# Kernel optimization log

Hardware: AMD Instinct MI355X
Metric: run time of the kernel (lower is better)

## Reference

```python
import jax, jax.numpy as jnp
import numpy as np

INPUT_DIM = 512
HIDDEN_DIM = 512


def setup_inputs() -> dict:
    key = jax.random.key(0)
    k1, k2 = jax.random.split(key, 2)
    T, B = 2048, 32
    x = jax.random.normal(k1, (T, B, INPUT_DIM), dtype=jnp.float32)
    hidden_state = jnp.zeros((1, B, HIDDEN_DIM), dtype=jnp.float32)
    cell_state = jnp.zeros((1, B, HIDDEN_DIM), dtype=jnp.float32)
    # xavier_uniform for weights, zeros for bias (matches init_weights)
    dim_size = INPUT_DIM + HIDDEN_DIM
    limit = np.sqrt(6.0 / (dim_size + 4 * HIDDEN_DIM)).astype(np.float32)
    weights = jax.random.uniform(k2, (dim_size, 4 * HIDDEN_DIM), dtype=jnp.float32,
                                 minval=-limit, maxval=limit)
    bias = jnp.zeros((4 * HIDDEN_DIM,), dtype=jnp.float32)
    return {"x": x, "hidden_state": hidden_state, "cell_state": cell_state,
            "weights": weights, "bias": bias}


def reference(x, hidden_state, cell_state, weights, bias):
    H = HIDDEN_DIM

    def step(carry, x_t):
        h, c = carry  # [1, B, H] each; x_t: [B, input_dim]
        concat = jnp.concatenate((x_t[None], h), axis=2)  # [1, B, in+H]
        gates = jnp.matmul(concat, weights) + bias        # [1, B, 4H]
        f = jax.nn.sigmoid(gates[:, :, :H])
        i = jax.nn.sigmoid(gates[:, :, H:2 * H])
        g = jnp.tanh(gates[:, :, 2 * H:3 * H])
        o = jax.nn.sigmoid(gates[:, :, 3 * H:])
        c_new = f * c + i * g
        h_new = o * jnp.tanh(c_new)
        return (h_new, c_new), h_new[0]  # emit [B, H]

    (h_f, c_f), outs = jax.lax.scan(step, (hidden_state, cell_state), x)
    return outs, (h_f, c_f)
```

## Files before the change

### kernel.cpp

```cpp
#include <hip/hip_runtime.h>
#include <math.h>

#define T_STEPS 2048
#define BATCH   32
#define IN_DIM  512
#define H_DIM   512
#define G4      2048
#define NWG     16
#define NTHR    512
#define TC      512
#define NCHUNK  4
#define GLS     132

typedef __attribute__((ext_vector_type(8))) short short8;
typedef __attribute__((ext_vector_type(4))) float f32x4;
typedef __attribute__((ext_vector_type(4))) unsigned u32x4;

__device__ inline unsigned short f2bf(float f) {
    unsigned u = __builtin_bit_cast(unsigned, f);
    unsigned r = (u + 0x7FFFu + ((u >> 16) & 1u)) >> 16;
    return (unsigned short)r;
}
__device__ inline unsigned pack2(float a, float b) {
    return (unsigned)f2bf(a) | ((unsigned)f2bf(b) << 16);
}
__device__ inline float sigm(float v) { return 1.f / (1.f + expf(-v)); }

__global__ __launch_bounds__(256) void wt_kernel(const float* __restrict__ W,
                                                 unsigned short* __restrict__ Wt) {
    __shared__ unsigned short tile[32][33];
    const int n0 = blockIdx.x << 5, k0 = blockIdx.y << 5;
    const int tx = threadIdx.x & 31, ty = threadIdx.x >> 5;
    #pragma unroll
    for (int r = 0; r < 32; r += 8)
        tile[ty + r][tx] = f2bf(W[(size_t)(k0 + ty + r) * G4 + n0 + tx]);
    __syncthreads();
    #pragma unroll
    for (int r = 0; r < 32; r += 8)
        Wt[(size_t)(n0 + ty + r) * 1024 + k0 + tx] = tile[tx][ty + r];
}

__global__ void init_h(const float* __restrict__ h0, unsigned short* __restrict__ hb) {
    int i = blockIdx.x * 256 + threadIdx.x;
    hb[i] = f2bf(h0[i]);
}

__global__ __launch_bounds__(256) void xw_mfma(const float* __restrict__ x,
                                               const unsigned short* __restrict__ Wt,
                                               const float* __restrict__ bias,
                                               float* __restrict__ pre) {
    __shared__ unsigned short As[64][40];
    __shared__ unsigned short Bs[64][40];
    const int tid = threadIdx.x;
    const int w = tid >> 6, l = tid & 63;
    const int m0 = blockIdx.y << 6, n0 = blockIdx.x << 6;
    const int srow = tid >> 2, sseg = (tid & 3) << 3;
    const int arow = (w << 4) + (l & 15);
    const int kb = (l >> 4) << 3;
    f32x4 acc[4] = {};

    for (int kc = 0; kc < 16; ++kc) {
        const float* xs = x + (size_t)(m0 + srow) * IN_DIM + kc * 32 + sseg;
        float4 xa = *(const float4*)xs;
        float4 xb2 = *(const float4*)(xs + 4);
        int4 av;
        av.x = pack2(xa.x, xa.y);  av.y = pack2(xa.z, xa.w);
        av.z = pack2(xb2.x, xb2.y); av.w = pack2(xb2.z, xb2.w);
        *(int4*)&As[srow][sseg] = av;
        *(int4*)&Bs[srow][sseg] = *(const int4*)(Wt + (size_t)(n0 + srow) * 1024 + kc * 32 + sseg);
        __syncthreads();
        short8 af = *(const short8*)&As[arow][kb];
        #pragma unroll
        for (int n = 0; n < 4; ++n) {
            short8 bf = *(const short8*)&Bs[(n << 4) + (l & 15)][kb];
            acc[n] = __builtin_amdgcn_mfma_f32_16x16x32_bf16(af, bf, acc[n], 0, 0, 0);
        }
        __syncthreads();
    }
    #pragma unroll
    for (int n = 0; n < 4; ++n) {
        const int col = n0 + (n << 4) + (l & 15);
        const float bb = bias[col];
        #pragma unroll
        for (int ri = 0; ri < 4; ++ri) {
            const int row = m0 + (w << 4) + ((l >> 4) << 2) + ri;
            pre[(size_t)row * G4 + col] = acc[n][ri] + bb;
        }
    }
}

__global__ __launch_bounds__(NTHR, 2) void lstm_scan(
        const unsigned short* __restrict__ Wt,
        const float* __restrict__ pre,
        const float* __restrict__ cin,
        float* __restrict__ cout,
        unsigned short* __restrict__ hbuf,
        float* __restrict__ outs,
        float* __restrict__ hf, float* __restrict__ cf,
        unsigned int* __restrict__ bar,
        int gt0) {
    __shared__ char Hl[32768];
    const int g = blockIdx.x;
    const int tid = threadIdx.x;
    const int w = tid >> 6, l = tid & 63;

    const int gc = ((w >> 1) << 9) + (g << 5) + ((w & 1) << 4) + (l & 15);
    short8 wf[16];
    #pragma unroll
    for (int kc = 0; kc < 16; ++kc)
        wf[kc] = *(const short8*)(Wt + (size_t)gc * 1024 + 512 + kc * 32 + ((l >> 4) << 3));

    const int b   = tid >> 4;
    const int hcp = (tid & 15) << 1;
    const int col = (g << 5) + hcp;
    float2 cv = *(const float2*)(cin + (b << 9) + col);

    const int arow0 = l & 15, arow1 = (l & 15) + 16;
    const int kbyte = (l >> 4) << 4;
    const int lcw = (w << 4) + (l & 15);
    const char* HlRd0 = Hl + arow0 * 1024;
    const char* HlRd1 = Hl + arow1 * 1024;
    const int swz0 = (arow0 & 7) << 4, swz1 = (arow1 & 7) << 4;
    __syncthreads();

    for (int t = 0; t < TC; ++t) {
        const int gt = gt0 + t;

        const float* pr = pre + ((size_t)t * BATCH + b) * G4 + col;
        const float2 pf = *(const float2*)pr;
        const float2 pi = *(const float2*)(pr + 512);
        const float2 pg = *(const float2*)(pr + 1024);
        const float2 po = *(const float2*)(pr + 1536);

        {
            const unsigned short* hsrc = hbuf + ((gt & 1) << 14);
            const unsigned short* hp0 = hsrc + (w << 9) + (l << 3);
            u32x4 v0, v1, v2, v3;
            asm volatile(
                "global_load_dwordx4 %0, %4, off sc1\n\t"
                "global_load_dwordx4 %1, %5, off sc1\n\t"
                "global_load_dwordx4 %2, %6, off sc1\n\t"
                "global_load_dwordx4 %3, %7, off sc1\n\t"
                "s_waitcnt vmcnt(0)"
                : "=&v"(v0), "=&v"(v1), "=&v"(v2), "=&v"(v3)
                : "v"(hp0), "v"(hp0 + 4096), "v"(hp0 + 8192), "v"(hp0 + 12288)
                : "memory");
            char* ld = Hl + w * 1024 + ((l << 4) ^ (w << 4));
            *(u32x4*)(ld)         = v0;
            *(u32x4*)(ld + 8192)  = v1;
            *(u32x4*)(ld + 16384) = v2;
            *(u32x4*)(ld + 24576) = v3;
        }
        __syncthreads();

        f32x4 acc0 = {0.f, 0.f, 0.f, 0.f}, acc1 = {0.f, 0.f, 0.f, 0.f};
        #pragma unroll
        for (int kc = 0; kc < 16; ++kc) {
            const int kb2 = kc * 64 + kbyte;
            short8 a0 = *(const short8*)(HlRd0 + (kb2 ^ swz0));
            short8 a1 = *(const short8*)(HlRd1 + (kb2 ^ swz1));
            acc0 = __builtin_amdgcn_mfma_f32_16x16x32_bf16(a0, wf[kc], acc0, 0, 0, 0);
            acc1 = __builtin_amdgcn_mfma_f32_16x16x32_bf16(a1, wf[kc], acc1, 0, 0, 0);
        }
        __syncthreads();
        float* Gl = (float*)Hl;
        #pragma unroll
        for (int ri = 0; ri < 4; ++ri) {
            const int br = ((l >> 4) << 2) + ri;
            Gl[br * GLS + lcw] = acc0[ri];
            Gl[(br + 16) * GLS + lcw] = acc1[ri];
        }
        __syncthreads();

        const float* grow = Gl + b * GLS + hcp;
        const float f0 = sigm(grow[0]  + pf.x), f1 = sigm(grow[1]  + pf.y);
        const float i0 = sigm(grow[32] + pi.x), i1 = sigm(grow[33] + pi.y);
        const float g0 = tanhf(grow[64] + pg.x), g1 = tanhf(grow[65] + pg.y);
        const float o0 = sigm(grow[96] + po.x), o1 = sigm(grow[97] + po.y);
        cv.x = f0 * cv.x + i0 * g0;
        cv.y = f1 * cv.y + i1 * g1;
        const float hn0 = o0 * tanhf(cv.x);
        const float hn1 = o1 * tanhf(cv.y);

        *(float2*)(outs + (size_t)gt * (BATCH * H_DIM) + (b << 9) + col) =
            make_float2(hn0, hn1);
        {
            unsigned* hdst = (unsigned*)(hbuf + (((gt + 1) & 1) << 14)) + (((b << 9) + col) >> 1);
            const unsigned pk = pack2(hn0, hn1);
            asm volatile("global_store_dword %0, %1, off sc1" :: "v"(hdst), "v"(pk) : "memory");
        }
        if (gt == T_STEPS - 1) {
            *(float2*)(hf + (b << 9) + col) = make_float2(hn0, hn1);
            *(float2*)(cf + (b << 9) + col) = make_float2(cv.x, cv.y);
        }

        asm volatile("s_waitcnt vmcnt(0)" ::: "memory");
        __syncthreads();
        if (tid == 0) {
            atomicAdd(bar, 1u);
            const unsigned tgt = (unsigned)(gt + 1) * NWG;
            for (;;) {
                unsigned vb;
                asm volatile("global_load_dword %0, %1, off sc1\n\ts_waitcnt vmcnt(0)"
                             : "=v"(vb) : "v"(bar) : "memory");
                if (vb >= tgt) break;
                __builtin_amdgcn_s_sleep(1);
            }
        }
        __syncthreads();
    }

    cout[(b << 9) + col]     = cv.x;
    cout[(b << 9) + col + 1] = cv.y;
}

__global__ __launch_bounds__(256) void lstm_step(const float* __restrict__ x_t,
                                                 const float* __restrict__ h_prev,
                                                 const float* __restrict__ W,
                                                 const float* __restrict__ bias,
                                                 const float* __restrict__ c_in,
                                                 float* __restrict__ c_out,
                                                 float* __restrict__ h_out,
                                                 float* __restrict__ hf,
                                                 float* __restrict__ cf, int last) {
    const int tid = threadIdx.x;
    const int hcc = tid & 7, b = tid >> 3;
    const int col = blockIdx.x * 8 + hcc;
    float a0 = bias[col], a1 = bias[col + 512], a2 = bias[col + 1024], a3 = bias[col + 1536];
    const float* xr = x_t + (size_t)b * IN_DIM;
    const float* hr = h_prev + (size_t)b * H_DIM;
    for (int k = 0; k < IN_DIM; ++k) {
        const float v = xr[k];
        const float* wk = &W[(size_t)k * G4 + col];
        a0 += v * wk[0]; a1 += v * wk[512]; a2 += v * wk[1024]; a3 += v * wk[1536];
    }
    for (int k = 0; k < H_DIM; ++k) {
        const float v = hr[k];
        const float* wk = &W[(size_t)(512 + k) * G4 + col];
        a0 += v * wk[0]; a1 += v * wk[512]; a2 += v * wk[1024]; a3 += v * wk[1536];
    }
    const float cn = sigm(a0) * c_in[(size_t)b * H_DIM + col] + sigm(a1) * tanhf(a2);
    const float hn = sigm(a3) * tanhf(cn);
    c_out[(size_t)b * H_DIM + col] = cn;
    h_out[(size_t)b * H_DIM + col] = hn;
    if (last) { hf[(size_t)b * H_DIM + col] = hn; cf[(size_t)b * H_DIM + col] = cn; }
}

extern "C" void kernel_launch(void* const* d_in, const int* in_sizes, int n_in,
                              void* d_out, int out_size, void* d_ws, size_t ws_size,
                              hipStream_t stream) {
    const float* x    = (const float*)d_in[0];
    const float* h0   = (const float*)d_in[1];
    const float* c0   = (const float*)d_in[2];
    const float* W    = (const float*)d_in[3];
    const float* bias = (const float*)d_in[4];

    float* outs = (float*)d_out;
    float* hf   = outs + (size_t)T_STEPS * BATCH * H_DIM;
    float* cf   = hf + BATCH * H_DIM;

    const size_t OFF_WT  = 134217728ull;
    const size_t OFF_HB  = OFF_WT + 4194304ull;
    const size_t OFF_C   = OFF_HB + 65536ull;
    const size_t OFF_BAR = OFF_C + 65536ull;
    const size_t NEED    = OFF_BAR + 4096ull;

    if (ws_size >= NEED) {
        float* pre = (float*)d_ws;
        unsigned short* Wt = (unsigned short*)((char*)d_ws + OFF_WT);
        unsigned short* hb = (unsigned short*)((char*)d_ws + OFF_HB);
        float* c_ws        = (float*)((char*)d_ws + OFF_C);
        unsigned int* bar  = (unsigned int*)((char*)d_ws + OFF_BAR);

        hipMemsetAsync(bar, 0, 64, stream);
        wt_kernel<<<dim3(64, 32), 256, 0, stream>>>(W, Wt);
        init_h<<<64, 256, 0, stream>>>(h0, hb);
        for (int k = 0; k < NCHUNK; ++k) {
            xw_mfma<<<dim3(32, TC * BATCH / 64), 256, 0, stream>>>(
                x + (size_t)k * TC * BATCH * IN_DIM, Wt, bias, pre);
            lstm_scan<<<NWG, NTHR, 0, stream>>>(
                Wt, pre, (k == 0) ? c0 : c_ws, c_ws, hb, outs, hf, cf, bar, k * TC);
        }
    } else {
        float* c_ws = (float*)d_ws;
        for (int t = 0; t < T_STEPS; ++t) {
            const float* hp = t ? outs + (size_t)(t - 1) * BATCH * H_DIM : h0;
            const float* ci = t ? c_ws : c0;
            lstm_step<<<64, 256, 0, stream>>>(x + (size_t)t * BATCH * IN_DIM,
                                              hp, W, bias, ci, c_ws,
                                              outs + (size_t)t * BATCH * H_DIM,
                                              hf, cf, (t == T_STEPS - 1) ? 1 : 0);
        }
    }
}
```

Baseline: 8.969 ms.

## Fuse input projection into persistent LSTM scan with prefetched bf16 x tiles

Removes the separate xW GEMM and its large fp32 pre-activation buffer. The recurrent kernel now holds both the input and the recurrent weight fragments in registers and does the x_t·W_x MFMAs inside each step. The next step's bf16 x tile is loaded from global memory during the current step and staged into LDS. The scan becomes a single launch over all timesteps instead of four chunks. The cost is doubled MFMA work on the serial critical path and higher register and LDS pressure, with occupancy dropped to one block per CU.

```diff
diff --git a/kernel.cpp b/kernel.cpp
--- a/kernel.cpp
+++ b/kernel.cpp
@@ -8,8 +8,6 @@
 #define G4      2048
 #define NWG     16
 #define NTHR    512
-#define TC      512
-#define NCHUNK  4
 #define GLS     132
 
 typedef __attribute__((ext_vector_type(8))) short short8;
@@ -25,6 +23,19 @@
     return (unsigned)f2bf(a) | ((unsigned)f2bf(b) << 16);
 }
 __device__ inline float sigm(float v) { return 1.f / (1.f + expf(-v)); }
+
+__device__ inline void ld4x_ic(const void* p0, const void* p1,
+                               const void* p2, const void* p3,
+                               u32x4& v0, u32x4& v1, u32x4& v2, u32x4& v3) {
+    asm volatile(
+        "global_load_dwordx4 %0, %4, off sc1\n\t"
+        "global_load_dwordx4 %1, %5, off sc1\n\t"
+        "global_load_dwordx4 %2, %6, off sc1\n\t"
+        "global_load_dwordx4 %3, %7, off sc1\n\t"
+        "s_waitcnt vmcnt(0)"
+        : "=&v"(v0), "=&v"(v1), "=&v"(v2), "=&v"(v3)
+        : "v"(p0), "v"(p1), "v"(p2), "v"(p3) : "memory");
+}
 
 __global__ __launch_bounds__(256) void wt_kernel(const float* __restrict__ W,
                                                  unsigned short* __restrict__ Wt) {
@@ -45,124 +56,97 @@
     hb[i] = f2bf(h0[i]);
 }
 
-__global__ __launch_bounds__(256) void xw_mfma(const float* __restrict__ x,
-                                               const unsigned short* __restrict__ Wt,
-                                               const float* __restrict__ bias,
-                                               float* __restrict__ pre) {
-    __shared__ unsigned short As[64][40];
-    __shared__ unsigned short Bs[64][40];
-    const int tid = threadIdx.x;
-    const int w = tid >> 6, l = tid & 63;
-    const int m0 = blockIdx.y << 6, n0 = blockIdx.x << 6;
-    const int srow = tid >> 2, sseg = (tid & 3) << 3;
-    const int arow = (w << 4) + (l & 15);
-    const int kb = (l >> 4) << 3;
-    f32x4 acc[4] = {};
-
-    for (int kc = 0; kc < 16; ++kc) {
-        const float* xs = x + (size_t)(m0 + srow) * IN_DIM + kc * 32 + sseg;
-        float4 xa = *(const float4*)xs;
-        float4 xb2 = *(const float4*)(xs + 4);
-        int4 av;
-        av.x = pack2(xa.x, xa.y);  av.y = pack2(xa.z, xa.w);
-        av.z = pack2(xb2.x, xb2.y); av.w = pack2(xb2.z, xb2.w);
-        *(int4*)&As[srow][sseg] = av;
-        *(int4*)&Bs[srow][sseg] = *(const int4*)(Wt + (size_t)(n0 + srow) * 1024 + kc * 32 + sseg);
-        __syncthreads();
-        short8 af = *(const short8*)&As[arow][kb];
-        #pragma unroll
-        for (int n = 0; n < 4; ++n) {
-            short8 bf = *(const short8*)&Bs[(n << 4) + (l & 15)][kb];
-            acc[n] = __builtin_amdgcn_mfma_f32_16x16x32_bf16(af, bf, acc[n], 0, 0, 0);
-        }
-        __syncthreads();
-    }
-    #pragma unroll
-    for (int n = 0; n < 4; ++n) {
-        const int col = n0 + (n << 4) + (l & 15);
-        const float bb = bias[col];
-        #pragma unroll
-        for (int ri = 0; ri < 4; ++ri) {
-            const int row = m0 + (w << 4) + ((l >> 4) << 2) + ri;
-            pre[(size_t)row * G4 + col] = acc[n][ri] + bb;
-        }
-    }
-}
-
-__global__ __launch_bounds__(NTHR, 2) void lstm_scan(
+__global__ __launch_bounds__(256) void xb_kernel(const float* __restrict__ x,
+                                                 unsigned short* __restrict__ xb) {
+    const size_t i = ((size_t)blockIdx.x * 256 + threadIdx.x) * 8;
+    const float4 a = *(const float4*)(x + i);
+    const float4 b = *(const float4*)(x + i + 4);
+    u32x4 v;
+    v.x = pack2(a.x, a.y); v.y = pack2(a.z, a.w);
+    v.z = pack2(b.x, b.y); v.w = pack2(b.z, b.w);
+    *(u32x4*)(xb + i) = v;
+}
+
+__global__ __launch_bounds__(NTHR, 1) void lstm_scan(
         const unsigned short* __restrict__ Wt,
-        const float* __restrict__ pre,
-        const float* __restrict__ cin,
-        float* __restrict__ cout,
+        const unsigned short* __restrict__ xb,
+        const float* __restrict__ bias,
+        const float* __restrict__ c0,
         unsigned short* __restrict__ hbuf,
         float* __restrict__ outs,
         float* __restrict__ hf, float* __restrict__ cf,
-        unsigned int* __restrict__ bar,
-        int gt0) {
-    __shared__ char Hl[32768];
+        unsigned int* __restrict__ bar) {
+    __shared__ char LDS_[65536];
+    char* Hl = LDS_;
+    char* Xl = LDS_ + 32768;
+
     const int g = blockIdx.x;
     const int tid = threadIdx.x;
     const int w = tid >> 6, l = tid & 63;
 
     const int gc = ((w >> 1) << 9) + (g << 5) + ((w & 1) << 4) + (l & 15);
-    short8 wf[16];
+    const int ksub = (l >> 4) << 3;
+    short8 wfh[16], wfx[16];
     #pragma unroll
-    for (int kc = 0; kc < 16; ++kc)
-        wf[kc] = *(const short8*)(Wt + (size_t)gc * 1024 + 512 + kc * 32 + ((l >> 4) << 3));
+    for (int kc = 0; kc < 16; ++kc) {
+        wfh[kc] = *(const short8*)(Wt + (size_t)gc * 1024 + 512 + kc * 32 + ksub);
+        wfx[kc] = *(const short8*)(Wt + (size_t)gc * 1024 +       kc * 32 + ksub);
+    }
+    const float bb = bias[gc];
 
     const int b   = tid >> 4;
     const int hcp = (tid & 15) << 1;
     const int col = (g << 5) + hcp;
-    float2 cv = *(const float2*)(cin + (b << 9) + col);
+    float2 cv = *(const float2*)(c0 + (b << 9) + col);
 
     const int arow0 = l & 15, arow1 = (l & 15) + 16;
     const int kbyte = (l >> 4) << 4;
+    const int swz0 = (arow0 & 7) << 4, swz1 = (arow1 & 7) << 4;
     const int lcw = (w << 4) + (l & 15);
-    const char* HlRd0 = Hl + arow0 * 1024;
-    const char* HlRd1 = Hl + arow1 * 1024;
-    const int swz0 = (arow0 & 7) << 4, swz1 = (arow1 & 7) << 4;
+
+    {
+        const u32x4* xsrc = (const u32x4*)xb;
+        u32x4 p0 = xsrc[(w << 6) + l], p1 = xsrc[(w << 6) + l + 512];
+        u32x4 p2 = xsrc[(w << 6) + l + 1024], p3 = xsrc[(w << 6) + l + 1536];
+        char* xd = Xl + w * 1024 + ((l << 4) ^ (w << 4));
+        *(u32x4*)xd = p0; *(u32x4*)(xd + 8192) = p1;
+        *(u32x4*)(xd + 16384) = p2; *(u32x4*)(xd + 24576) = p3;
+
+        const unsigned short* hp0 = hbuf + (w << 9) + (l << 3);
+        u32x4 v0, v1, v2, v3;
+        ld4x_ic(hp0, hp0 + 4096, hp0 + 8192, hp0 + 12288, v0, v1, v2, v3);
+        char* hd = Hl + w * 1024 + ((l << 4) ^ (w << 4));
+        *(u32x4*)hd = v0; *(u32x4*)(hd + 8192) = v1;
+        *(u32x4*)(hd + 16384) = v2; *(u32x4*)(hd + 24576) = v3;
+    }
     __syncthreads();
 
-    for (int t = 0; t < TC; ++t) {
-        const int gt = gt0 + t;
-
-        const float* pr = pre + ((size_t)t * BATCH + b) * G4 + col;
-        const float2 pf = *(const float2*)pr;
-        const float2 pi = *(const float2*)(pr + 512);
-        const float2 pg = *(const float2*)(pr + 1024);
-        const float2 po = *(const float2*)(pr + 1536);
-
-        {
-            const unsigned short* hsrc = hbuf + ((gt & 1) << 14);
-            const unsigned short* hp0 = hsrc + (w << 9) + (l << 3);
-            u32x4 v0, v1, v2, v3;
-            asm volatile(
-                "global_load_dwordx4 %0, %4, off sc1\n\t"
-                "global_load_dwordx4 %1, %5, off sc1\n\t"
-                "global_load_dwordx4 %2, %6, off sc1\n\t"
-                "global_load_dwordx4 %3, %7, off sc1\n\t"
-                "s_waitcnt vmcnt(0)"
-                : "=&v"(v0), "=&v"(v1), "=&v"(v2), "=&v"(v3)
-                : "v"(hp0), "v"(hp0 + 4096), "v"(hp0 + 8192), "v"(hp0 + 12288)
-                : "memory");
-            char* ld = Hl + w * 1024 + ((l << 4) ^ (w << 4));
-            *(u32x4*)(ld)         = v0;
-            *(u32x4*)(ld + 8192)  = v1;
-            *(u32x4*)(ld + 16384) = v2;
-            *(u32x4*)(ld + 24576) = v3;
-        }
-        __syncthreads();
-
-        f32x4 acc0 = {0.f, 0.f, 0.f, 0.f}, acc1 = {0.f, 0.f, 0.f, 0.f};
+    for (int gt = 0; gt < T_STEPS; ++gt) {
+        const int gtn = (gt < T_STEPS - 1) ? gt + 1 : gt;
+        const u32x4* xsrc = (const u32x4*)(xb + ((size_t)gtn << 14));
+        const u32x4 px0 = xsrc[(w << 6) + l];
+        const u32x4 px1 = xsrc[(w << 6) + l + 512];
+        const u32x4 px2 = xsrc[(w << 6) + l + 1024];
+        const u32x4 px3 = xsrc[(w << 6) + l + 1536];
+
+        f32x4 ah0 = {bb, bb, bb, bb}, ah1 = {bb, bb, bb, bb};
+        f32x4 ax0 = {0.f, 0.f, 0.f, 0.f}, ax1 = {0.f, 0.f, 0.f, 0.f};
         #pragma unroll
         for (int kc = 0; kc < 16; ++kc) {
             const int kb2 = kc * 64 + kbyte;
-            short8 a0 = *(const short8*)(HlRd0 + (kb2 ^ swz0));
-            short8 a1 = *(const short8*)(HlRd1 + (kb2 ^ swz1));
-            acc0 = __builtin_amdgcn_mfma_f32_16x16x32_bf16(a0, wf[kc], acc0, 0, 0, 0);
-            acc1 = __builtin_amdgcn_mfma_f32_16x16x32_bf16(a1, wf[kc], acc1, 0, 0, 0);
-        }
-        __syncthreads();
+            short8 ha0 = *(const short8*)(Hl + arow0 * 1024 + (kb2 ^ swz0));
+            short8 ha1 = *(const short8*)(Hl + arow1 * 1024 + (kb2 ^ swz1));
+            short8 qa0 = *(const short8*)(Xl + arow0 * 1024 + (kb2 ^ swz0));
+            short8 qa1 = *(const short8*)(Xl + arow1 * 1024 + (kb2 ^ swz1));
+            ah0 = __builtin_amdgcn_mfma_f32_16x16x32_bf16(ha0, wfh[kc], ah0, 0, 0, 0);
+            ax0 = __builtin_amdgcn_mfma_f32_16x16x32_bf16(qa0, wfx[kc], ax0, 0, 0, 0);
+            ah1 = __builtin_amdgcn_mfma_f32_16x16x32_bf16(ha1, wfh[kc], ah1, 0, 0, 0);
+            ax1 = __builtin_amdgcn_mfma_f32_16x16x32_bf16(qa1, wfx[kc], ax1, 0, 0, 0);
+        }
+        const f32x4 acc0 = ah0 + ax0;
+        const f32x4 acc1 = ah1 + ax1;
+        __syncthreads();
+
         float* Gl = (float*)Hl;
         #pragma unroll
         for (int ri = 0; ri < 4; ++ri) {
@@ -170,28 +154,33 @@
             Gl[br * GLS + lcw] = acc0[ri];
             Gl[(br + 16) * GLS + lcw] = acc1[ri];
         }
+        {
+            char* xd = Xl + w * 1024 + ((l << 4) ^ (w << 4));
+            *(u32x4*)xd = px0; *(u32x4*)(xd + 8192) = px1;
+            *(u32x4*)(xd + 16384) = px2; *(u32x4*)(xd + 24576) = px3;
+        }
         __syncthreads();
 
         const float* grow = Gl + b * GLS + hcp;
-        const float f0 = sigm(grow[0]  + pf.x), f1 = sigm(grow[1]  + pf.y);
-        const float i0 = sigm(grow[32] + pi.x), i1 = sigm(grow[33] + pi.y);
-        const float g0 = tanhf(grow[64] + pg.x), g1 = tanhf(grow[65] + pg.y);
-        const float o0 = sigm(grow[96] + po.x), o1 = sigm(grow[97] + po.y);
+        const float f0 = sigm(grow[0]),   f1 = sigm(grow[1]);
+        const float i0 = sigm(grow[32]),  i1 = sigm(grow[33]);
+        const float g0 = tanhf(grow[64]), g1 = tanhf(grow[65]);
+        const float o0 = sigm(grow[96]),  o1 = sigm(grow[97]);
         cv.x = f0 * cv.x + i0 * g0;
         cv.y = f1 * cv.y + i1 * g1;
         const float hn0 = o0 * tanhf(cv.x);
         const float hn1 = o1 * tanhf(cv.y);
 
-        *(float2*)(outs + (size_t)gt * (BATCH * H_DIM) + (b << 9) + col) =
-            make_float2(hn0, hn1);
+        *(float2*)(outs + ((size_t)gt << 14) + (b << 9) + col) = make_float2(hn0, hn1);
         {
-            unsigned* hdst = (unsigned*)(hbuf + (((gt + 1) & 1) << 14)) + (((b << 9) + col) >> 1);
+            unsigned* hdst = (unsigned*)hbuf + (((gt + 1) & 1) << 13) + (b << 8) + (col >> 1);
             const unsigned pk = pack2(hn0, hn1);
             asm volatile("global_store_dword %0, %1, off sc1" :: "v"(hdst), "v"(pk) : "memory");
         }
         if (gt == T_STEPS - 1) {
             *(float2*)(hf + (b << 9) + col) = make_float2(hn0, hn1);
             *(float2*)(cf + (b << 9) + col) = make_float2(cv.x, cv.y);
+            break;
         }
 
         asm volatile("s_waitcnt vmcnt(0)" ::: "memory");
@@ -208,10 +197,17 @@
             }
         }
         __syncthreads();
-    }
-
-    cout[(b << 9) + col]     = cv.x;
-    cout[(b << 9) + col + 1] = cv.y;
+
+        {
+            const unsigned short* hsrc = hbuf + (((gt + 1) & 1) << 14) + (w << 9) + (l << 3);
+            u32x4 v0, v1, v2, v3;
+            ld4x_ic(hsrc, hsrc + 4096, hsrc + 8192, hsrc + 12288, v0, v1, v2, v3);
+            char* hd = Hl + w * 1024 + ((l << 4) ^ (w << 4));
+            *(u32x4*)hd = v0; *(u32x4*)(hd + 8192) = v1;
+            *(u32x4*)(hd + 16384) = v2; *(u32x4*)(hd + 24576) = v3;
+        }
+        __syncthreads();
+    }
 }
 
 __global__ __launch_bounds__(256) void lstm_step(const float* __restrict__ x_t,
@@ -259,28 +255,22 @@
     float* hf   = outs + (size_t)T_STEPS * BATCH * H_DIM;
     float* cf   = hf + BATCH * H_DIM;
 
-    const size_t OFF_WT  = 134217728ull;
-    const size_t OFF_HB  = OFF_WT + 4194304ull;
-    const size_t OFF_C   = OFF_HB + 65536ull;
-    const size_t OFF_BAR = OFF_C + 65536ull;
-    const size_t NEED    = OFF_BAR + 4096ull;
+    const size_t OFF_WT = 67108864ull;
+    const size_t OFF_HB = OFF_WT + 4194304ull;
+    const size_t OFF_BA = OFF_HB + 65536ull;
+    const size_t NEED   = OFF_BA + 4096ull;
 
     if (ws_size >= NEED) {
-        float* pre = (float*)d_ws;
+        unsigned short* xb = (unsigned short*)d_ws;
         unsigned short* Wt = (unsigned short*)((char*)d_ws + OFF_WT);
         unsigned short* hb = (unsigned short*)((char*)d_ws + OFF_HB);
-        float* c_ws        = (float*)((char*)d_ws + OFF_C);
-        unsigned int* bar  = (unsigned int*)((char*)d_ws + OFF_BAR);
-
-        hipMemsetAsync(bar, 0, 64, stream);
+        unsigned int* bar  = (unsigned int*)((char*)d_ws + OFF_BA);
+
+        hipMemsetAsync(bar, 0, 256, stream);
         wt_kernel<<<dim3(64, 32), 256, 0, stream>>>(W, Wt);
         init_h<<<64, 256, 0, stream>>>(h0, hb);
-        for (int k = 0; k < NCHUNK; ++k) {
-            xw_mfma<<<dim3(32, TC * BATCH / 64), 256, 0, stream>>>(
-                x + (size_t)k * TC * BATCH * IN_DIM, Wt, bias, pre);
-            lstm_scan<<<NWG, NTHR, 0, stream>>>(
-                Wt, pre, (k == 0) ? c0 : c_ws, c_ws, hb, outs, hf, cf, bar, k * TC);
-        }
+        xb_kernel<<<16384, 256, 0, stream>>>(x, xb);
+        lstm_scan<<<NWG, NTHR, 0, stream>>>(Wt, xb, bias, c0, hb, outs, hf, cf, bar);
     } else {
         float* c_ws = (float*)d_ws;
         for (int t = 0; t < T_STEPS; ++t) {
```

After: 10.44 ms. 1.16x slower.
